# Kernel optimization log

Hardware: AMD Instinct MI355X
Metric: run time of the kernel (lower is better)

Reference implementation:

```python
import jax, jax.numpy as jnp
import numpy as np

N, F, H, C, E = 100000, 64, 128, 10, 1600000
BN_EPS = 1e-5


def setup_inputs() -> dict:
    key = jax.random.key(0)
    ks = jax.random.split(key, 16)
    s = 0.05
    return {
        "x": jax.random.normal(ks[0], (N, F), dtype=jnp.float32),
        "edge_index": jax.random.randint(ks[1], (2, E), 0, N, dtype=jnp.int64),
        # conv1 MLP: Linear(F,H), ReLU, Linear(H,H)
        "w1a": jax.random.normal(ks[2], (F, H), dtype=jnp.float32) * s,
        "b1a": jnp.zeros((H,), jnp.float32),
        "w1b": jax.random.normal(ks[3], (H, H), dtype=jnp.float32) * s,
        "b1b": jnp.zeros((H,), jnp.float32),
        # conv2 MLP: Linear(H,H), ReLU, Linear(H,H)
        "w2a": jax.random.normal(ks[4], (H, H), dtype=jnp.float32) * s,
        "b2a": jnp.zeros((H,), jnp.float32),
        "w2b": jax.random.normal(ks[5], (H, H), dtype=jnp.float32) * s,
        "b2b": jnp.zeros((H,), jnp.float32),
        # BatchNorm affine params
        "bn1_g": jnp.ones((H,), jnp.float32),
        "bn1_b": jnp.zeros((H,), jnp.float32),
        "bn2_g": jnp.ones((H,), jnp.float32),
        "bn2_b": jnp.zeros((H,), jnp.float32),
        # classifier MLP: Linear(H,H), ReLU, (Dropout=identity), Linear(H,C)
        "mw1": jax.random.normal(ks[6], (H, H), dtype=jnp.float32) * s,
        "mb1": jnp.zeros((H,), jnp.float32),
        "mw2": jax.random.normal(ks[7], (H, C), dtype=jnp.float32) * s,
        "mb2": jnp.zeros((C,), jnp.float32),
    }


def _gin_conv(x, src, dst, wa, ba, wb, bb):
    # GINConv, eps=0: mlp( sum_{j in N(i)} x_j + x_i )
    agg = jax.ops.segment_sum(x[src], dst, num_segments=N) + x
    h = jax.nn.relu(agg @ wa + ba)
    return h @ wb + bb


def _batchnorm(h, g, b):
    mean = jnp.mean(h, axis=0)
    var = jnp.var(h, axis=0)  # biased, matches torch BN training normalization
    return (h - mean) * jax.lax.rsqrt(var + BN_EPS) * g + b


def reference(x, edge_index, w1a, b1a, w1b, b1b, w2a, b2a, w2b, b2b,
              bn1_g, bn1_b, bn2_g, bn2_b, mw1, mb1, mw2, mb2):
    src, dst = edge_index[0], edge_index[1]
    h = _gin_conv(x, src, dst, w1a, b1a, w1b, b1b)
    h = jax.nn.relu(_batchnorm(h, bn1_g, bn1_b))
    h = _gin_conv(h, src, dst, w2a, b2a, w2b, b2b)
    latent = jax.nn.relu(_batchnorm(h, bn2_g, bn2_b))
    # classifier (dropout = identity at inference)
    m = jax.nn.relu(latent @ mw1 + mb1)
    class_out = m @ mw2 + mb2
    return latent, class_out
```

## Files before the change

### kernel.cpp

```cpp
#include <hip/hip_runtime.h>
#include <cstdint>


#define NN 100000
#define FF 64
#define HH 128
#define CC 10
#define EE 1600000
#define BN_EPS 1e-5f
#define MBLK 128
#define NBLK_LIN ((NN + MBLK - 1) / MBLK)
#define BSHIFT 7
#define NBUCK ((NN + 127) / 128)
#define CHUNK 16384
#define NB_CH ((EE + CHUNK - 1) / CHUNK)
#define NB_CVT 3125
#define TW (8192 + 4 * 16384 + 2048)
#define TWB ((TW + 255) / 256)

typedef __attribute__((ext_vector_type(8))) short bf16x8;
typedef __attribute__((ext_vector_type(4))) float f32x4;

__device__ inline unsigned short f2bf(float f) {
    unsigned int u = __float_as_uint(f);
    unsigned int r = (u + 0x7fffu + ((u >> 16) & 1u)) >> 16;
    return (unsigned short)r;
}
__device__ inline float b2f(unsigned short h) {
    return __uint_as_float(((unsigned int)h) << 16);
}
__device__ inline unsigned int pack2(float a, float b) {
    return (unsigned int)f2bf(a) | ((unsigned int)f2bf(b) << 16);
}
__device__ inline int detect_i64(const unsigned int* e) {
    return (e[1] | e[3] | e[5] | e[7]) == 0u;
}
__device__ inline int edge_dst(const void* eiv, int f, int e) {
    return f ? (int)((const long long*)eiv)[EE + e] : ((const int*)eiv)[EE + e];
}
__device__ inline int edge_src(const void* eiv, int f, int e) {
    return f ? (int)((const long long*)eiv)[e] : ((const int*)eiv)[e];
}

__global__ __launch_bounds__(256) void cvtprep_kernel(
    const float* __restrict__ x, unsigned short* __restrict__ xb,
    const float* __restrict__ w1a, const float* __restrict__ w1b,
    const float* __restrict__ w2a, const float* __restrict__ w2b,
    const float* __restrict__ mw1, const float* __restrict__ mw2,
    unsigned short* __restrict__ wt1a, unsigned short* __restrict__ wt1b,
    unsigned short* __restrict__ wt2a, unsigned short* __restrict__ wt2b,
    unsigned short* __restrict__ wtm1, unsigned short* __restrict__ wtm2,
    float* __restrict__ stats, int* __restrict__ gbcount) {
    const int tid = threadIdx.x;
    const int b = blockIdx.x;
    if (b == 0) {
        for (int i = tid; i < 512; i += 256) stats[i] = 0.f;
        for (int i = tid; i < NBUCK; i += 256) gbcount[i] = 0;
    }
    if (b < NB_CVT) {
        int i = b * 256 + tid;
        float4 a = ((const float4*)x)[i * 2];
        float4 c = ((const float4*)x)[i * 2 + 1];
        uint4 o;
        o.x = pack2(a.x, a.y); o.y = pack2(a.z, a.w);
        o.z = pack2(c.x, c.y); o.w = pack2(c.z, c.w);
        ((uint4*)xb)[i] = o;
        return;
    }
    int idx = (b - NB_CVT) * 256 + tid;
    if (idx < 8192) {
        int k = idx >> 7, n = idx & 127;
        wt1a[n * 64 + k] = f2bf(w1a[idx]);
    } else if (idx < 8192 + 16384) {
        int t = idx - 8192; int k = t >> 7, n = t & 127;
        wt1b[n * 128 + k] = f2bf(w1b[t]);
    } else if (idx < 8192 + 2 * 16384) {
        int t = idx - (8192 + 16384); int k = t >> 7, n = t & 127;
        wt2a[n * 128 + k] = f2bf(w2a[t]);
    } else if (idx < 8192 + 3 * 16384) {
        int t = idx - (8192 + 2 * 16384); int k = t >> 7, n = t & 127;
        wt2b[n * 128 + k] = f2bf(w2b[t]);
    } else if (idx < 8192 + 4 * 16384) {
        int t = idx - (8192 + 3 * 16384); int k = t >> 7, n = t & 127;
        wtm1[n * 128 + k] = f2bf(mw1[t]);
    } else if (idx < TW) {
        int t = idx - (8192 + 4 * 16384); int n = t & 15, k = t >> 4;
        wtm2[n * 128 + k] = (n < CC) ? f2bf(mw2[k * CC + n]) : (unsigned short)0;
    }
}

__global__ __launch_bounds__(256) void p1_hist_kernel(const void* __restrict__ eiv,
                                                      int* __restrict__ gbcount) {
    __shared__ int hist[NBUCK];
    const int tid = threadIdx.x;
    const int f = detect_i64((const unsigned int*)eiv);
    for (int i = tid; i < NBUCK; i += 256) hist[i] = 0;
    __syncthreads();
    int beg = blockIdx.x * CHUNK, end = min(beg + CHUNK, EE);
    for (int e = beg + tid; e < end; e += 256)
        atomicAdd(&hist[edge_dst(eiv, f, e) >> BSHIFT], 1);
    __syncthreads();
    for (int i = tid; i < NBUCK; i += 256)
        if (hist[i]) atomicAdd(&gbcount[i], hist[i]);
}

__global__ __launch_bounds__(1024) void bscan_kernel(const int* __restrict__ gbcount,
                                                     int* __restrict__ gbstart,
                                                     int* __restrict__ gbcursor,
                                                     int* __restrict__ rowstart) {
    __shared__ int s[1024];
    const int tid = threadIdx.x;
    int v = (tid < NBUCK) ? gbcount[tid] : 0;
    s[tid] = v;
    __syncthreads();
    for (int off = 1; off < 1024; off <<= 1) {
        int t = (tid >= off) ? s[tid - off] : 0;
        __syncthreads();
        s[tid] += t;
        __syncthreads();
    }
    if (tid < NBUCK) {
        int e = s[tid] - v;
        gbstart[tid] = e;
        gbcursor[tid] = e;
    }
    if (tid == 0) { gbstart[NBUCK] = EE; rowstart[NN] = EE; }
}

__global__ __launch_bounds__(256) void p2_bin_kernel(const void* __restrict__ eiv,
                                                     int* __restrict__ gbcursor,
                                                     unsigned int* __restrict__ packed) {
    __shared__ int hist[NBUCK];
    __shared__ int basep[NBUCK];
    const int tid = threadIdx.x;
    const int f = detect_i64((const unsigned int*)eiv);
    for (int i = tid; i < NBUCK; i += 256) hist[i] = 0;
    __syncthreads();
    int beg = blockIdx.x * CHUNK, end = min(beg + CHUNK, EE);
    for (int e = beg + tid; e < end; e += 256)
        atomicAdd(&hist[edge_dst(eiv, f, e) >> BSHIFT], 1);
    __syncthreads();
    for (int i = tid; i < NBUCK; i += 256) {
        int c = hist[i];
        if (c) basep[i] = atomicAdd(&gbcursor[i], c);
        hist[i] = 0;
    }
    __syncthreads();
    for (int e = beg + tid; e < end; e += 256) {
        int s = edge_src(eiv, f, e);
        int d = edge_dst(eiv, f, e);
        int b = d >> BSHIFT;
        int r = atomicAdd(&hist[b], 1);
        packed[basep[b] + r] = (unsigned int)s | ((unsigned int)(d & 127) << 17);
    }
}

__global__ __launch_bounds__(256) void p3_sort_kernel(const unsigned int* __restrict__ packed,
                                                      const int* __restrict__ gbstart,
                                                      int* __restrict__ rowstart,
                                                      int* __restrict__ eidx) {
    __shared__ int hist[128];
    __shared__ int excl[128];
    __shared__ int s[128];
    const int tid = threadIdx.x;
    const int b = blockIdx.x;
    const int bstart = gbstart[b], bend = gbstart[b + 1];
    if (tid < 128) hist[tid] = 0;
    __syncthreads();
    for (int e = bstart + tid; e < bend; e += 256)
        atomicAdd(&hist[packed[e] >> 17], 1);
    __syncthreads();
    int v = (tid < 128) ? hist[tid] : 0;
    if (tid < 128) s[tid] = v;
    __syncthreads();
    for (int off = 1; off < 128; off <<= 1) {
        int t = (tid < 128 && tid >= off) ? s[tid - off] : 0;
        __syncthreads();
        if (tid < 128) s[tid] += t;
        __syncthreads();
    }
    if (tid < 128) {
        excl[tid] = s[tid] - v;
        hist[tid] = 0;
        int node = b * 128 + tid;
        if (node < NN) rowstart[node] = bstart + excl[tid];
    }
    __syncthreads();
    for (int e = bstart + tid; e < bend; e += 256) {
        unsigned int p = packed[e];
        int dl = p >> 17;
        int r = atomicAdd(&hist[dl], 1);
        eidx[bstart + excl[dl] + r] = (int)(p & 0x1FFFFu);
    }
}

template <int FDIM, int BN>
__global__ __launch_bounds__(256) void gather_kernel(const unsigned short* __restrict__ src,
                                                     const int* __restrict__ rowstart,
                                                     const int* __restrict__ eidx,
                                                     const float* __restrict__ statsum,
                                                     const float* __restrict__ statsq,
                                                     const float* __restrict__ bng,
                                                     const float* __restrict__ bnb,
                                                     unsigned short* __restrict__ agg) {
    constexpr int LPN = FDIM / 2;
    constexpr int NPB = 256 / LPN;
    int node = blockIdx.x * NPB + threadIdx.x / LPN;
    int lane2 = threadIdx.x % LPN;
    if (node >= NN) return;
    const int c = lane2 * 2;
    float s0c = 1.f, s1c = 1.f, o0c = 0.f, o1c = 0.f;
    if (BN) {
        float m0 = statsum[c] * (1.0f / NN);
        float m1 = statsum[c + 1] * (1.0f / NN);
        float v0 = statsq[c] * (1.0f / NN) - m0 * m0;
        float v1 = statsq[c + 1] * (1.0f / NN) - m1 * m1;
        s0c = bng[c] * rsqrtf(v0 + BN_EPS);
        s1c = bng[c + 1] * rsqrtf(v1 + BN_EPS);
        o0c = bnb[c] - m0 * s0c;
        o1c = bnb[c + 1] - m1 * s1c;
    }
    float ax = 0.f, ay = 0.f;
    auto addv = [&](unsigned int v) {
        float f0 = b2f((unsigned short)(v & 0xffff));
        float f1 = b2f((unsigned short)(v >> 16));
        if (BN) {
            f0 = fmaxf(fmaf(f0, s0c, o0c), 0.f);
            f1 = fmaxf(fmaf(f1, s1c, o1c), 0.f);
        }
        ax += f0; ay += f1;
    };
    addv(*(const unsigned int*)(src + (size_t)node * FDIM + c));
    int beg = rowstart[node], end = rowstart[node + 1];
    int j = beg;
    for (; j + 7 < end; j += 8) {
        int i0 = eidx[j],     i1 = eidx[j + 1], i2 = eidx[j + 2], i3 = eidx[j + 3];
        int i4 = eidx[j + 4], i5 = eidx[j + 5], i6 = eidx[j + 6], i7 = eidx[j + 7];
        unsigned int v0 = *(const unsigned int*)(src + (size_t)i0 * FDIM + c);
        unsigned int v1 = *(const unsigned int*)(src + (size_t)i1 * FDIM + c);
        unsigned int v2 = *(const unsigned int*)(src + (size_t)i2 * FDIM + c);
        unsigned int v3 = *(const unsigned int*)(src + (size_t)i3 * FDIM + c);
        unsigned int v4 = *(const unsigned int*)(src + (size_t)i4 * FDIM + c);
        unsigned int v5 = *(const unsigned int*)(src + (size_t)i5 * FDIM + c);
        unsigned int v6 = *(const unsigned int*)(src + (size_t)i6 * FDIM + c);
        unsigned int v7 = *(const unsigned int*)(src + (size_t)i7 * FDIM + c);
        addv(v0); addv(v1); addv(v2); addv(v3);
        addv(v4); addv(v5); addv(v6); addv(v7);
    }
    for (; j < end; j++)
        addv(*(const unsigned int*)(src + (size_t)eidx[j] * FDIM + c));
    *(unsigned int*)(agg + (size_t)node * FDIM + c) = pack2(ax, ay);
}

template <int KIN>
__global__ __launch_bounds__(256) void mlp_kernel(const unsigned short* __restrict__ in,
                                                  const unsigned short* __restrict__ wTa,
                                                  const float* __restrict__ ba,
                                                  const unsigned short* __restrict__ wTb,
                                                  const float* __restrict__ bb,
                                                  unsigned short* __restrict__ out,
                                                  float* __restrict__ bnsum,
                                                  float* __restrict__ bnsq) {
    constexpr int KLDA = KIN + 8;
    constexpr int CH = KIN / 8;
    __shared__ __attribute__((aligned(16))) unsigned short sA[MBLK * 136];
    __shared__ __attribute__((aligned(16))) unsigned short sW[128 * 136];
    __shared__ float sSt[256];
    __shared__ float sB[256];

    const int tid = threadIdx.x;
    const int wave = tid >> 6, lane = tid & 63;
    const int quad = lane >> 4, l16 = lane & 15;
    const long long row0 = (long long)blockIdx.x * MBLK;

    sSt[tid] = 0.f;
    if (tid < 128) sB[tid] = ba[tid];
    else sB[tid] = bb[tid - 128];

    for (int i = tid; i < 128 * CH; i += 256)
        *(uint4*)(sW + (i / CH) * KLDA + (i % CH) * 8) = ((const uint4*)wTa)[i];
    for (int i = tid; i < MBLK * CH; i += 256) {
        int r = i / CH, c = i % CH;
        uint4 v = {0u, 0u, 0u, 0u};
        if (row0 + r < NN) v = *(const uint4*)(in + (row0 + r) * KIN + c * 8);
        *(uint4*)(sA + r * KLDA + c * 8) = v;
    }
    __syncthreads();

    f32x4 acc1[2][8];
#pragma unroll
    for (int t = 0; t < 2; t++)
#pragma unroll
        for (int n = 0; n < 8; n++) acc1[t][n] = 0.f;
#pragma unroll
    for (int ks = 0; ks < KIN / 32; ks++) {
        bf16x8 a0 = *(const bf16x8*)(sA + (wave * 32 + l16) * KLDA + ks * 32 + quad * 8);
        bf16x8 a1 = *(const bf16x8*)(sA + (wave * 32 + 16 + l16) * KLDA + ks * 32 + quad * 8);
#pragma unroll
        for (int nt = 0; nt < 8; nt++) {
            bf16x8 b = *(const bf16x8*)(sW + (nt * 16 + l16) * KLDA + ks * 32 + quad * 8);
            acc1[0][nt] = __builtin_amdgcn_mfma_f32_16x16x32_bf16(a0, b, acc1[0][nt], 0, 0, 0);
            acc1[1][nt] = __builtin_amdgcn_mfma_f32_16x16x32_bf16(a1, b, acc1[1][nt], 0, 0, 0);
        }
    }
    __syncthreads();

#pragma unroll
    for (int nt = 0; nt < 8; nt++) {
        const int col = nt * 16 + l16;
        const float bcol = sB[col];
#pragma unroll
        for (int t = 0; t < 2; t++)
#pragma unroll
            for (int r = 0; r < 4; r++) {
                int rl = wave * 32 + t * 16 + quad * 4 + r;
                sA[rl * 136 + col] = f2bf(fmaxf(acc1[t][nt][r] + bcol, 0.f));
            }
    }
    for (int i = tid; i < 128 * 16; i += 256)
        *(uint4*)(sW + (i >> 4) * 136 + (i & 15) * 8) = ((const uint4*)wTb)[i];
    __syncthreads();

    f32x4 acc2[2][8];
#pragma unroll
    for (int t = 0; t < 2; t++)
#pragma unroll
        for (int n = 0; n < 8; n++) acc2[t][n] = 0.f;
#pragma unroll
    for (int ks = 0; ks < 4; ks++) {
        bf16x8 a0 = *(const bf16x8*)(sA + (wave * 32 + l16) * 136 + ks * 32 + quad * 8);
        bf16x8 a1 = *(const bf16x8*)(sA + (wave * 32 + 16 + l16) * 136 + ks * 32 + quad * 8);
#pragma unroll
        for (int nt = 0; nt < 8; nt++) {
            bf16x8 b = *(const bf16x8*)(sW + (nt * 16 + l16) * 136 + ks * 32 + quad * 8);
            acc2[0][nt] = __builtin_amdgcn_mfma_f32_16x16x32_bf16(a0, b, acc2[0][nt], 0, 0, 0);
            acc2[1][nt] = __builtin_amdgcn_mfma_f32_16x16x32_bf16(a1, b, acc2[1][nt], 0, 0, 0);
        }
    }
    __syncthreads();

#pragma unroll
    for (int nt = 0; nt < 8; nt++) {
        const int col = nt * 16 + l16;
        const float bcol = sB[128 + col];
        float ls = 0.f, lq = 0.f;
#pragma unroll
        for (int t = 0; t < 2; t++)
#pragma unroll
            for (int r = 0; r < 4; r++) {
                int rl = wave * 32 + t * 16 + quad * 4 + r;
                float v = acc2[t][nt][r] + bcol;
                if (row0 + rl < NN) { ls += v; lq += v * v; }
                sA[rl * 136 + col] = f2bf(v);
            }
        ls += __shfl_down(ls, 32); ls += __shfl_down(ls, 16);
        lq += __shfl_down(lq, 32); lq += __shfl_down(lq, 16);
        if (lane < 16) { atomicAdd(&sSt[col], ls); atomicAdd(&sSt[128 + col], lq); }
    }
    __syncthreads();

    for (int i = tid; i < MBLK * 16; i += 256) {
        int r = i >> 4, c = i & 15;
        if (row0 + r < NN)
            *(uint4*)(out + (row0 + r) * 128 + c * 8) = *(const uint4*)(sA + r * 136 + c * 8);
    }
    if (tid < 128) atomicAdd(&bnsum[tid], sSt[tid]);
    else atomicAdd(&bnsq[tid - 128], sSt[tid]);
}

__global__ __launch_bounds__(256) void final_kernel(const unsigned short* __restrict__ h2,
                                                    const float* __restrict__ statsum,
                                                    const float* __restrict__ statsq,
                                                    const float* __restrict__ bng,
                                                    const float* __restrict__ bnb,
                                                    const unsigned short* __restrict__ wTm1,
                                                    const float* __restrict__ mb1,
                                                    const unsigned short* __restrict__ wTm2,
                                                    const float* __restrict__ mb2,
                                                    float* __restrict__ latent,
                                                    float* __restrict__ cls) {
    __shared__ __attribute__((aligned(16))) unsigned short sA[MBLK * 136];
    __shared__ __attribute__((aligned(16))) unsigned short sW[128 * 136];
    __shared__ float sBN[256];
    __shared__ float sB1[128];

    const int tid = threadIdx.x;
    const int wave = tid >> 6, lane = tid & 63;
    const int quad = lane >> 4, l16 = lane & 15;
    const long long row0 = (long long)blockIdx.x * MBLK;

    if (tid < 128) {
        float mean = statsum[tid] * (1.0f / NN);
        float var = statsq[tid] * (1.0f / NN) - mean * mean;
        float sc = bng[tid] * rsqrtf(var + BN_EPS);
        sBN[tid] = sc;
        sBN[128 + tid] = bnb[tid] - mean * sc;
        sB1[tid] = mb1[tid];
    }
    for (int i = tid; i < 128 * 16; i += 256)
        *(uint4*)(sW + (i >> 4) * 136 + (i & 15) * 8) = ((const uint4*)wTm1)[i];
    __syncthreads();

    for (int i = tid; i < MBLK * 16; i += 256) {
        int r = i >> 4, c = i & 15;
        bool live = (row0 + r < NN);
        uint4 hv = {0u, 0u, 0u, 0u};
        if (live) hv = *(const uint4*)(h2 + (row0 + r) * 128 + c * 8);
        const unsigned int* wv = (const unsigned int*)&hv;
        float vs[8];
#pragma unroll
        for (int p = 0; p < 4; p++) {
            int cc = c * 8 + p * 2;
            vs[p * 2]     = fmaxf(fmaf(b2f((unsigned short)(wv[p] & 0xffff)), sBN[cc], sBN[128 + cc]), 0.f);
            vs[p * 2 + 1] = fmaxf(fmaf(b2f((unsigned short)(wv[p] >> 16)), sBN[cc + 1], sBN[129 + cc]), 0.f);
        }
        if (live) {
            float4 f0 = {vs[0], vs[1], vs[2], vs[3]};
            float4 f1 = {vs[4], vs[5], vs[6], vs[7]};
            float* lp = latent + (row0 + r) * 128 + c * 8;
            *(float4*)lp = f0;
            *(float4*)(lp + 4) = f1;
        }
        uint4 o;
        o.x = pack2(vs[0], vs[1]); o.y = pack2(vs[2], vs[3]);
        o.z = pack2(vs[4], vs[5]); o.w = pack2(vs[6], vs[7]);
        *(uint4*)(sA + r * 136 + c * 8) = o;
    }
    __syncthreads();

    f32x4 acc1[2][8];
#pragma unroll
    for (int t = 0; t < 2; t++)
#pragma unroll
        for (int n = 0; n < 8; n++) acc1[t][n] = 0.f;
#pragma unroll
    for (int ks = 0; ks < 4; ks++) {
        bf16x8 av0 = *(const bf16x8*)(sA + (wave * 32 + l16) * 136 + ks * 32 + quad * 8);
        bf16x8 av1 = *(const bf16x8*)(sA + (wave * 32 + 16 + l16) * 136 + ks * 32 + quad * 8);
#pragma unroll
        for (int nt = 0; nt < 8; nt++) {
            bf16x8 b = *(const bf16x8*)(sW + (nt * 16 + l16) * 136 + ks * 32 + quad * 8);
            acc1[0][nt] = __builtin_amdgcn_mfma_f32_16x16x32_bf16(av0, b, acc1[0][nt], 0, 0, 0);
            acc1[1][nt] = __builtin_amdgcn_mfma_f32_16x16x32_bf16(av1, b, acc1[1][nt], 0, 0, 0);
        }
    }
    __syncthreads();

#pragma unroll
    for (int nt = 0; nt < 8; nt++) {
        const int col = nt * 16 + l16;
        const float bcol = sB1[col];
#pragma unroll
        for (int t = 0; t < 2; t++)
#pragma unroll
            for (int r = 0; r < 4; r++) {
                int rl = wave * 32 + t * 16 + quad * 4 + r;
                sA[rl * 136 + col] = f2bf(fmaxf(acc1[t][nt][r] + bcol, 0.f));
            }
    }
    if (tid < 256)
        *(uint4*)(sW + (tid >> 4) * 136 + (tid & 15) * 8) = ((const uint4*)wTm2)[tid];
    __syncthreads();

    f32x4 acc2[2];
    acc2[0] = 0.f; acc2[1] = 0.f;
#pragma unroll
    for (int ks = 0; ks < 4; ks++) {
        bf16x8 av0 = *(const bf16x8*)(sA + (wave * 32 + l16) * 136 + ks * 32 + quad * 8);
        bf16x8 av1 = *(const bf16x8*)(sA + (wave * 32 + 16 + l16) * 136 + ks * 32 + quad * 8);
        bf16x8 b = *(const bf16x8*)(sW + l16 * 136 + ks * 32 + quad * 8);
        acc2[0] = __builtin_amdgcn_mfma_f32_16x16x32_bf16(av0, b, acc2[0], 0, 0, 0);
        acc2[1] = __builtin_amdgcn_mfma_f32_16x16x32_bf16(av1, b, acc2[1], 0, 0, 0);
    }
    __syncthreads();

    float* sOf = (float*)sA;
    if (l16 < CC) {
        const float bc = mb2[l16];
#pragma unroll
        for (int t = 0; t < 2; t++)
#pragma unroll
            for (int r = 0; r < 4; r++) {
                int rl = wave * 32 + t * 16 + quad * 4 + r;
                sOf[rl * CC + l16] = acc2[t][r] + bc;
            }
    }
    __syncthreads();
    for (int i = tid; i < MBLK * CC; i += 256) {
        long long gi = row0 * CC + i;
        if (gi < (long long)NN * CC) cls[gi] = sOf[i];
    }
}

extern "C" void kernel_launch(void* const* d_in, const int* in_sizes, int n_in,
                              void* d_out, int out_size, void* d_ws, size_t ws_size,
                              hipStream_t stream) {
    const float* x   = (const float*)d_in[0];
    const void* ei   = d_in[1];
    const float* w1a = (const float*)d_in[2];
    const float* b1a = (const float*)d_in[3];
    const float* w1b = (const float*)d_in[4];
    const float* b1b = (const float*)d_in[5];
    const float* w2a = (const float*)d_in[6];
    const float* b2a = (const float*)d_in[7];
    const float* w2b = (const float*)d_in[8];
    const float* b2b = (const float*)d_in[9];
    const float* bn1g = (const float*)d_in[10];
    const float* bn1b = (const float*)d_in[11];
    const float* bn2g = (const float*)d_in[12];
    const float* bn2b = (const float*)d_in[13];
    const float* mw1 = (const float*)d_in[14];
    const float* mb1 = (const float*)d_in[15];
    const float* mw2 = (const float*)d_in[16];
    const float* mb2 = (const float*)d_in[17];
    float* out = (float*)d_out;

    char* w = (char*)d_ws;
    unsigned short* xb   = (unsigned short*)w;  w += (size_t)NN * FF * 2;
    unsigned short* agg1 = (unsigned short*)w;  w += (size_t)NN * FF * 2;
    unsigned short* h    = (unsigned short*)w;  w += (size_t)NN * HH * 2;
    unsigned short* agg2 = (unsigned short*)w;  w += (size_t)NN * HH * 2;
    float* stats = (float*)w;                   w += 1024 * 4;
    int* eidx = (int*)w;                        w += (size_t)EE * 4;
    unsigned int* packed = (unsigned int*)w;    w += (size_t)EE * 4;
    int* rowstart = (int*)w;                    w += (NN + 2) * 4;
    int* gbcount = (int*)w;                     w += (NBUCK + 2) * 4;
    int* gbstart = (int*)w;                     w += (NBUCK + 2) * 4;
    int* gbcursor = (int*)w;                    w += (NBUCK + 2) * 4;
    unsigned short* wt1a = (unsigned short*)w;  w += 8192 * 2;
    unsigned short* wt1b = (unsigned short*)w;  w += 16384 * 2;
    unsigned short* wt2a = (unsigned short*)w;  w += 16384 * 2;
    unsigned short* wt2b = (unsigned short*)w;  w += 16384 * 2;
    unsigned short* wtm1 = (unsigned short*)w;  w += 16384 * 2;
    unsigned short* wtm2 = (unsigned short*)w;  w += 2048 * 2;

    cvtprep_kernel<<<NB_CVT + TWB, 256, 0, stream>>>(
        x, xb, w1a, w1b, w2a, w2b, mw1, mw2,
        wt1a, wt1b, wt2a, wt2b, wtm1, wtm2, stats, gbcount);

    p1_hist_kernel<<<NB_CH, 256, 0, stream>>>(ei, gbcount);
    bscan_kernel<<<1, 1024, 0, stream>>>(gbcount, gbstart, gbcursor, rowstart);
    p2_bin_kernel<<<NB_CH, 256, 0, stream>>>(ei, gbcursor, packed);
    p3_sort_kernel<<<NBUCK, 256, 0, stream>>>(packed, gbstart, rowstart, eidx);

    gather_kernel<FF, 0><<<(NN + 7) / 8, 256, 0, stream>>>(
        xb, rowstart, eidx, nullptr, nullptr, nullptr, nullptr, agg1);
    mlp_kernel<FF><<<NBLK_LIN, 256, 0, stream>>>(agg1, wt1a, b1a, wt1b, b1b, h, stats, stats + 128);

    gather_kernel<HH, 1><<<(NN + 3) / 4, 256, 0, stream>>>(
        h, rowstart, eidx, stats, stats + 128, bn1g, bn1b, agg2);
    mlp_kernel<HH><<<NBLK_LIN, 256, 0, stream>>>(agg2, wt2a, b2a, wt2b, b2b, h, stats + 256, stats + 384);

    final_kernel<<<NBLK_LIN, 256, 0, stream>>>(
        h, stats + 256, stats + 384, bn2g, bn2b,
        wtm1, mb1, wtm2, mb2, out, out + (size_t)NN * HH);
}
```

Baseline: 408.9 us.

## Fuse edge histogram into prep, per-chunk offsets, fuse sort with first gather

```diff
diff --git a/kernel.cpp b/kernel.cpp
--- a/kernel.cpp
+++ b/kernel.cpp
@@ -17,6 +17,7 @@
 #define NB_CVT 3125
 #define TW (8192 + 4 * 16384 + 2048)
 #define TWB ((TW + 255) / 256)
+#define LDSE 3072
 
 typedef __attribute__((ext_vector_type(8))) short bf16x8;
 typedef __attribute__((ext_vector_type(4))) float f32x4;
@@ -50,13 +51,13 @@
     unsigned short* __restrict__ wt1a, unsigned short* __restrict__ wt1b,
     unsigned short* __restrict__ wt2a, unsigned short* __restrict__ wt2b,
     unsigned short* __restrict__ wtm1, unsigned short* __restrict__ wtm2,
-    float* __restrict__ stats, int* __restrict__ gbcount) {
+    float* __restrict__ stats, const void* __restrict__ eiv,
+    int* __restrict__ chunkhist) {
+    __shared__ int hist[NBUCK];
     const int tid = threadIdx.x;
     const int b = blockIdx.x;
-    if (b == 0) {
+    if (b == 0)
         for (int i = tid; i < 512; i += 256) stats[i] = 0.f;
-        for (int i = tid; i < NBUCK; i += 256) gbcount[i] = 0;
-    }
     if (b < NB_CVT) {
         int i = b * 256 + tid;
         float4 a = ((const float4*)x)[i * 2];
@@ -67,46 +68,59 @@
         ((uint4*)xb)[i] = o;
         return;
     }
-    int idx = (b - NB_CVT) * 256 + tid;
-    if (idx < 8192) {
-        int k = idx >> 7, n = idx & 127;
-        wt1a[n * 64 + k] = f2bf(w1a[idx]);
-    } else if (idx < 8192 + 16384) {
-        int t = idx - 8192; int k = t >> 7, n = t & 127;
-        wt1b[n * 128 + k] = f2bf(w1b[t]);
-    } else if (idx < 8192 + 2 * 16384) {
-        int t = idx - (8192 + 16384); int k = t >> 7, n = t & 127;
-        wt2a[n * 128 + k] = f2bf(w2a[t]);
-    } else if (idx < 8192 + 3 * 16384) {
-        int t = idx - (8192 + 2 * 16384); int k = t >> 7, n = t & 127;
-        wt2b[n * 128 + k] = f2bf(w2b[t]);
-    } else if (idx < 8192 + 4 * 16384) {
-        int t = idx - (8192 + 3 * 16384); int k = t >> 7, n = t & 127;
-        wtm1[n * 128 + k] = f2bf(mw1[t]);
-    } else if (idx < TW) {
-        int t = idx - (8192 + 4 * 16384); int n = t & 15, k = t >> 4;
-        wtm2[n * 128 + k] = (n < CC) ? f2bf(mw2[k * CC + n]) : (unsigned short)0;
-    }
-}
-
-__global__ __launch_bounds__(256) void p1_hist_kernel(const void* __restrict__ eiv,
-                                                      int* __restrict__ gbcount) {
-    __shared__ int hist[NBUCK];
-    const int tid = threadIdx.x;
+    if (b < NB_CVT + TWB) {
+        int idx = (b - NB_CVT) * 256 + tid;
+        if (idx < 8192) {
+            int k = idx >> 7, n = idx & 127;
+            wt1a[n * 64 + k] = f2bf(w1a[idx]);
+        } else if (idx < 8192 + 16384) {
+            int t = idx - 8192; int k = t >> 7, n = t & 127;
+            wt1b[n * 128 + k] = f2bf(w1b[t]);
+        } else if (idx < 8192 + 2 * 16384) {
+            int t = idx - (8192 + 16384); int k = t >> 7, n = t & 127;
+            wt2a[n * 128 + k] = f2bf(w2a[t]);
+        } else if (idx < 8192 + 3 * 16384) {
+            int t = idx - (8192 + 2 * 16384); int k = t >> 7, n = t & 127;
+            wt2b[n * 128 + k] = f2bf(w2b[t]);
+        } else if (idx < 8192 + 4 * 16384) {
+            int t = idx - (8192 + 3 * 16384); int k = t >> 7, n = t & 127;
+            wtm1[n * 128 + k] = f2bf(mw1[t]);
+        } else if (idx < TW) {
+            int t = idx - (8192 + 4 * 16384); int n = t & 15, k = t >> 4;
+            wtm2[n * 128 + k] = (n < CC) ? f2bf(mw2[k * CC + n]) : (unsigned short)0;
+        }
+        return;
+    }
+    const int ch = b - NB_CVT - TWB;
     const int f = detect_i64((const unsigned int*)eiv);
     for (int i = tid; i < NBUCK; i += 256) hist[i] = 0;
     __syncthreads();
-    int beg = blockIdx.x * CHUNK, end = min(beg + CHUNK, EE);
+    int beg = ch * CHUNK, end = min(beg + CHUNK, EE);
     for (int e = beg + tid; e < end; e += 256)
         atomicAdd(&hist[edge_dst(eiv, f, e) >> BSHIFT], 1);
     __syncthreads();
-    for (int i = tid; i < NBUCK; i += 256)
-        if (hist[i]) atomicAdd(&gbcount[i], hist[i]);
+    for (int i = tid; i < NBUCK; i += 256) chunkhist[ch * NBUCK + i] = hist[i];
+}
+
+__global__ __launch_bounds__(128) void chunkscan_kernel(int* __restrict__ chunkhist,
+                                                        int* __restrict__ gbcount) {
+    __shared__ int s[128];
+    const int b = blockIdx.x, tid = threadIdx.x;
+    int v = (tid < NB_CH) ? chunkhist[tid * NBUCK + b] : 0;
+    s[tid] = v;
+    __syncthreads();
+    for (int off = 1; off < 128; off <<= 1) {
+        int t = (tid >= off) ? s[tid - off] : 0;
+        __syncthreads();
+        s[tid] += t;
+        __syncthreads();
+    }
+    if (tid < NB_CH) chunkhist[tid * NBUCK + b] = s[tid] - v;
+    if (tid == 127) gbcount[b] = s[127];
 }
 
 __global__ __launch_bounds__(1024) void bscan_kernel(const int* __restrict__ gbcount,
                                                      int* __restrict__ gbstart,
-                                                     int* __restrict__ gbcursor,
                                                      int* __restrict__ rowstart) {
     __shared__ int s[1024];
     const int tid = threadIdx.x;
@@ -119,33 +133,25 @@
         s[tid] += t;
         __syncthreads();
     }
-    if (tid < NBUCK) {
-        int e = s[tid] - v;
-        gbstart[tid] = e;
-        gbcursor[tid] = e;
-    }
+    if (tid < NBUCK) gbstart[tid] = s[tid] - v;
     if (tid == 0) { gbstart[NBUCK] = EE; rowstart[NN] = EE; }
 }
 
 __global__ __launch_bounds__(256) void p2_bin_kernel(const void* __restrict__ eiv,
-                                                     int* __restrict__ gbcursor,
+                                                     const int* __restrict__ gbstart,
+                                                     const int* __restrict__ relbase,
                                                      unsigned int* __restrict__ packed) {
     __shared__ int hist[NBUCK];
     __shared__ int basep[NBUCK];
     const int tid = threadIdx.x;
+    const int ch = blockIdx.x;
     const int f = detect_i64((const unsigned int*)eiv);
-    for (int i = tid; i < NBUCK; i += 256) hist[i] = 0;
-    __syncthreads();
-    int beg = blockIdx.x * CHUNK, end = min(beg + CHUNK, EE);
-    for (int e = beg + tid; e < end; e += 256)
-        atomicAdd(&hist[edge_dst(eiv, f, e) >> BSHIFT], 1);
-    __syncthreads();
     for (int i = tid; i < NBUCK; i += 256) {
-        int c = hist[i];
-        if (c) basep[i] = atomicAdd(&gbcursor[i], c);
         hist[i] = 0;
-    }
-    __syncthreads();
+        basep[i] = gbstart[i] + relbase[ch * NBUCK + i];
+    }
+    __syncthreads();
+    int beg = ch * CHUNK, end = min(beg + CHUNK, EE);
     for (int e = beg + tid; e < end; e += 256) {
         int s = edge_src(eiv, f, e);
         int d = edge_dst(eiv, f, e);
@@ -155,101 +161,139 @@
     }
 }
 
-__global__ __launch_bounds__(256) void p3_sort_kernel(const unsigned int* __restrict__ packed,
-                                                      const int* __restrict__ gbstart,
-                                                      int* __restrict__ rowstart,
-                                                      int* __restrict__ eidx) {
+__global__ __launch_bounds__(256) void p3g1_kernel(const unsigned int* __restrict__ packed,
+                                                   const int* __restrict__ gbstart,
+                                                   const unsigned short* __restrict__ xb,
+                                                   int* __restrict__ rowstart,
+                                                   int* __restrict__ eidx,
+                                                   unsigned short* __restrict__ agg1) {
     __shared__ int hist[128];
     __shared__ int excl[128];
-    __shared__ int s[128];
+    __shared__ int sc[128];
+    __shared__ int lidx[LDSE];
     const int tid = threadIdx.x;
     const int b = blockIdx.x;
     const int bstart = gbstart[b], bend = gbstart[b + 1];
+    const int cnt = bend - bstart;
     if (tid < 128) hist[tid] = 0;
     __syncthreads();
     for (int e = bstart + tid; e < bend; e += 256)
         atomicAdd(&hist[packed[e] >> 17], 1);
     __syncthreads();
     int v = (tid < 128) ? hist[tid] : 0;
-    if (tid < 128) s[tid] = v;
+    if (tid < 128) sc[tid] = v;
     __syncthreads();
     for (int off = 1; off < 128; off <<= 1) {
-        int t = (tid < 128 && tid >= off) ? s[tid - off] : 0;
+        int t = (tid < 128 && tid >= off) ? sc[tid - off] : 0;
         __syncthreads();
-        if (tid < 128) s[tid] += t;
+        if (tid < 128) sc[tid] += t;
         __syncthreads();
     }
     if (tid < 128) {
-        excl[tid] = s[tid] - v;
+        excl[tid] = sc[tid] - v;
         hist[tid] = 0;
         int node = b * 128 + tid;
-        if (node < NN) rowstart[node] = bstart + excl[tid];
-    }
-    __syncthreads();
+        if (node < NN) rowstart[node] = bstart + sc[tid] - v;
+    }
+    __syncthreads();
+    const bool inl = (cnt <= LDSE);
     for (int e = bstart + tid; e < bend; e += 256) {
         unsigned int p = packed[e];
         int dl = p >> 17;
         int r = atomicAdd(&hist[dl], 1);
-        eidx[bstart + excl[dl] + r] = (int)(p & 0x1FFFFu);
-    }
-}
-
-template <int FDIM, int BN>
-__global__ __launch_bounds__(256) void gather_kernel(const unsigned short* __restrict__ src,
-                                                     const int* __restrict__ rowstart,
-                                                     const int* __restrict__ eidx,
-                                                     const float* __restrict__ statsum,
-                                                     const float* __restrict__ statsq,
-                                                     const float* __restrict__ bng,
-                                                     const float* __restrict__ bnb,
-                                                     unsigned short* __restrict__ agg) {
-    constexpr int LPN = FDIM / 2;
-    constexpr int NPB = 256 / LPN;
-    int node = blockIdx.x * NPB + threadIdx.x / LPN;
-    int lane2 = threadIdx.x % LPN;
+        int pos = excl[dl] + r;
+        int sv = (int)(p & 0x1FFFFu);
+        eidx[bstart + pos] = sv;
+        if (inl) lidx[pos] = sv;
+    }
+    __syncthreads();
+    const int* ep = inl ? (const int*)lidx : (eidx + bstart);
+    const int g = tid >> 3, l8 = tid & 7, c = l8 * 8;
+    for (int r4 = 0; r4 < 4; r4++) {
+        int nl = r4 * 32 + g;
+        int node = b * 128 + nl;
+        if (node >= NN) continue;
+        float acc[8];
+        uint4 sv4 = *(const uint4*)(xb + (size_t)node * FF + c);
+        {
+            const unsigned int* wv = (const unsigned int*)&sv4;
+#pragma unroll
+            for (int p = 0; p < 4; p++) {
+                acc[p * 2] = b2f((unsigned short)(wv[p] & 0xffff));
+                acc[p * 2 + 1] = b2f((unsigned short)(wv[p] >> 16));
+            }
+        }
+        auto addv = [&](uint4 u) {
+            const unsigned int* wv = (const unsigned int*)&u;
+#pragma unroll
+            for (int p = 0; p < 4; p++) {
+                acc[p * 2] += b2f((unsigned short)(wv[p] & 0xffff));
+                acc[p * 2 + 1] += b2f((unsigned short)(wv[p] >> 16));
+            }
+        };
+        int beg2 = excl[nl], cend = beg2 + hist[nl];
+        int j = beg2;
+        for (; j + 3 < cend; j += 4) {
+            int i0 = ep[j], i1 = ep[j + 1], i2 = ep[j + 2], i3 = ep[j + 3];
+            uint4 v0 = *(const uint4*)(xb + (size_t)i0 * FF + c);
+            uint4 v1 = *(const uint4*)(xb + (size_t)i1 * FF + c);
+            uint4 v2 = *(const uint4*)(xb + (size_t)i2 * FF + c);
+            uint4 v3 = *(const uint4*)(xb + (size_t)i3 * FF + c);
+            addv(v0); addv(v1); addv(v2); addv(v3);
+        }
+        for (; j < cend; j++)
+            addv(*(const uint4*)(xb + (size_t)ep[j] * FF + c));
+        uint4 o;
+        o.x = pack2(acc[0], acc[1]); o.y = pack2(acc[2], acc[3]);
+        o.z = pack2(acc[4], acc[5]); o.w = pack2(acc[6], acc[7]);
+        *(uint4*)(agg1 + (size_t)node * FF + c) = o;
+    }
+}
+
+__global__ __launch_bounds__(256) void gather2_kernel(const unsigned short* __restrict__ h,
+                                                      const int* __restrict__ rowstart,
+                                                      const int* __restrict__ eidx,
+                                                      const float* __restrict__ statsum,
+                                                      const float* __restrict__ statsq,
+                                                      const float* __restrict__ bng,
+                                                      const float* __restrict__ bnb,
+                                                      unsigned short* __restrict__ agg2) {
+    int node = blockIdx.x * 8 + (threadIdx.x >> 5);
+    const int l32 = threadIdx.x & 31;
+    const int c = l32 * 4;
     if (node >= NN) return;
-    const int c = lane2 * 2;
-    float s0c = 1.f, s1c = 1.f, o0c = 0.f, o1c = 0.f;
-    if (BN) {
-        float m0 = statsum[c] * (1.0f / NN);
-        float m1 = statsum[c + 1] * (1.0f / NN);
-        float v0 = statsq[c] * (1.0f / NN) - m0 * m0;
-        float v1 = statsq[c + 1] * (1.0f / NN) - m1 * m1;
-        s0c = bng[c] * rsqrtf(v0 + BN_EPS);
-        s1c = bng[c + 1] * rsqrtf(v1 + BN_EPS);
-        o0c = bnb[c] - m0 * s0c;
-        o1c = bnb[c + 1] - m1 * s1c;
-    }
-    float ax = 0.f, ay = 0.f;
-    auto addv = [&](unsigned int v) {
-        float f0 = b2f((unsigned short)(v & 0xffff));
-        float f1 = b2f((unsigned short)(v >> 16));
-        if (BN) {
-            f0 = fmaxf(fmaf(f0, s0c, o0c), 0.f);
-            f1 = fmaxf(fmaf(f1, s1c, o1c), 0.f);
-        }
-        ax += f0; ay += f1;
+    float scl[4], off[4];
+#pragma unroll
+    for (int k = 0; k < 4; k++) {
+        float m = statsum[c + k] * (1.0f / NN);
+        float vv = statsq[c + k] * (1.0f / NN) - m * m;
+        scl[k] = bng[c + k] * rsqrtf(vv + BN_EPS);
+        off[k] = bnb[c + k] - m * scl[k];
+    }
+    float acc[4] = {0.f, 0.f, 0.f, 0.f};
+    auto addv = [&](uint2 u) {
+        acc[0] += fmaxf(fmaf(b2f((unsigned short)(u.x & 0xffff)), scl[0], off[0]), 0.f);
+        acc[1] += fmaxf(fmaf(b2f((unsigned short)(u.x >> 16)), scl[1], off[1]), 0.f);
+        acc[2] += fmaxf(fmaf(b2f((unsigned short)(u.y & 0xffff)), scl[2], off[2]), 0.f);
+        acc[3] += fmaxf(fmaf(b2f((unsigned short)(u.y >> 16)), scl[3], off[3]), 0.f);
     };
-    addv(*(const unsigned int*)(src + (size_t)node * FDIM + c));
+    addv(*(const uint2*)(h + (size_t)node * HH + c));
     int beg = rowstart[node], end = rowstart[node + 1];
     int j = beg;
-    for (; j + 7 < end; j += 8) {
-        int i0 = eidx[j],     i1 = eidx[j + 1], i2 = eidx[j + 2], i3 = eidx[j + 3];
-        int i4 = eidx[j + 4], i5 = eidx[j + 5], i6 = eidx[j + 6], i7 = eidx[j + 7];
-        unsigned int v0 = *(const unsigned int*)(src + (size_t)i0 * FDIM + c);
-        unsigned int v1 = *(const unsigned int*)(src + (size_t)i1 * FDIM + c);
-        unsigned int v2 = *(const unsigned int*)(src + (size_t)i2 * FDIM + c);
-        unsigned int v3 = *(const unsigned int*)(src + (size_t)i3 * FDIM + c);
-        unsigned int v4 = *(const unsigned int*)(src + (size_t)i4 * FDIM + c);
-        unsigned int v5 = *(const unsigned int*)(src + (size_t)i5 * FDIM + c);
-        unsigned int v6 = *(const unsigned int*)(src + (size_t)i6 * FDIM + c);
-        unsigned int v7 = *(const unsigned int*)(src + (size_t)i7 * FDIM + c);
+    for (; j + 3 < end; j += 4) {
+        int i0 = eidx[j], i1 = eidx[j + 1], i2 = eidx[j + 2], i3 = eidx[j + 3];
+        uint2 v0 = *(const uint2*)(h + (size_t)i0 * HH + c);
+        uint2 v1 = *(const uint2*)(h + (size_t)i1 * HH + c);
+        uint2 v2 = *(const uint2*)(h + (size_t)i2 * HH + c);
+        uint2 v3 = *(const uint2*)(h + (size_t)i3 * HH + c);
         addv(v0); addv(v1); addv(v2); addv(v3);
-        addv(v4); addv(v5); addv(v6); addv(v7);
     }
     for (; j < end; j++)
-        addv(*(const unsigned int*)(src + (size_t)eidx[j] * FDIM + c));
-    *(unsigned int*)(agg + (size_t)node * FDIM + c) = pack2(ax, ay);
+        addv(*(const uint2*)(h + (size_t)eidx[j] * HH + c));
+    uint2 o;
+    o.x = pack2(acc[0], acc[1]);
+    o.y = pack2(acc[2], acc[3]);
+    *(uint2*)(agg2 + (size_t)node * HH + c) = o;
 }
 
 template <int KIN>
@@ -526,7 +570,7 @@
     int* rowstart = (int*)w;                    w += (NN + 2) * 4;
     int* gbcount = (int*)w;                     w += (NBUCK + 2) * 4;
     int* gbstart = (int*)w;                     w += (NBUCK + 2) * 4;
-    int* gbcursor = (int*)w;                    w += (NBUCK + 2) * 4;
+    int* chunkhist = (int*)w;                   w += (size_t)NB_CH * NBUCK * 4;
     unsigned short* wt1a = (unsigned short*)w;  w += 8192 * 2;
     unsigned short* wt1b = (unsigned short*)w;  w += 16384 * 2;
     unsigned short* wt2a = (unsigned short*)w;  w += 16384 * 2;
@@ -534,20 +578,19 @@
     unsigned short* wtm1 = (unsigned short*)w;  w += 16384 * 2;
     unsigned short* wtm2 = (unsigned short*)w;  w += 2048 * 2;
 
-    cvtprep_kernel<<<NB_CVT + TWB, 256, 0, stream>>>(
+    cvtprep_kernel<<<NB_CVT + TWB + NB_CH, 256, 0, stream>>>(
         x, xb, w1a, w1b, w2a, w2b, mw1, mw2,
-        wt1a, wt1b, wt2a, wt2b, wtm1, wtm2, stats, gbcount);
-
-    p1_hist_kernel<<<NB_CH, 256, 0, stream>>>(ei, gbcount);
-    bscan_kernel<<<1, 1024, 0, stream>>>(gbcount, gbstart, gbcursor, rowstart);
-    p2_bin_kernel<<<NB_CH, 256, 0, stream>>>(ei, gbcursor, packed);
-    p3_sort_kernel<<<NBUCK, 256, 0, stream>>>(packed, gbstart, rowstart, eidx);
-
-    gather_kernel<FF, 0><<<(NN + 7) / 8, 256, 0, stream>>>(
-        xb, rowstart, eidx, nullptr, nullptr, nullptr, nullptr, agg1);
+        wt1a, wt1b, wt2a, wt2b, wtm1, wtm2, stats, ei, chunkhist);
+
+    chunkscan_kernel<<<NBUCK, 128, 0, stream>>>(chunkhist, gbcount);
+    bscan_kernel<<<1, 1024, 0, stream>>>(gbcount, gbstart, rowstart);
+    p2_bin_kernel<<<NB_CH, 256, 0, stream>>>(ei, gbstart, chunkhist, packed);
+
+    p3g1_kernel<<<NBUCK, 256, 0, stream>>>(packed, gbstart, xb, rowstart, eidx, agg1);
+
     mlp_kernel<FF><<<NBLK_LIN, 256, 0, stream>>>(agg1, wt1a, b1a, wt1b, b1b, h, stats, stats + 128);
 
-    gather_kernel<HH, 1><<<(NN + 3) / 4, 256, 0, stream>>>(
+    gather2_kernel<<<(NN + 7) / 8, 256, 0, stream>>>(
         h, rowstart, eidx, stats, stats + 128, bn1g, bn1b, agg2);
     mlp_kernel<HH><<<NBLK_LIN, 256, 0, stream>>>(agg2, wt2a, b2a, wt2b, b2b, h, stats + 256, stats + 384);
 
```

Result: faster. 377.7 us, median of 2 (-7.6%).
